# Optimization experiments

Hardware: AMD Instinct MI355X
Metric: run time of the kernel (lower is better)

## Reference

```python
import jax, jax.numpy as jnp
import numpy as np

N = 10000; E = 320000
DIM = 176; ATT = 16; SH_HEADS = 16; TH = 4; NH = SH_HEADS + TH; VD = DIM // SH_HEADS
LMAX = 3; NSPH = (LMAX + 1) ** 2; ZDIM = 16; RDIM = 16
RSTART = 0.8; CUT = 5.0; NLAYERS = 2


def _ln(x):
    mu = jnp.mean(x, axis=-1, keepdims=True)
    dx = x - mu
    var = jnp.mean(dx ** 2, axis=-1, keepdims=True)
    return dx * (1e-6 + var) ** (-0.5)


def _sph(v):
    # real spherical harmonics up to l=3, unnormalized overall scale, [E,16]
    x, y, z = v[..., 0], v[..., 1], v[..., 2]
    s3 = np.float32(np.sqrt(3.0)); s15 = np.float32(np.sqrt(15.0))
    c1 = np.float32(np.sqrt(5.0 / 8.0)); c2 = np.float32(np.sqrt(3.0 / 8.0))
    x2, y2, z2 = x * x, y * y, z * z
    return jnp.stack([
        jnp.ones_like(x),
        x, y, z,
        s3 * x * y, s3 * y * z, 0.5 * (3.0 * z2 - 1.0), s3 * x * z, 0.5 * s3 * (x2 - y2),
        c1 * y * (3.0 * x2 - y2), s15 * x * y * z, c2 * y * (5.0 * z2 - 1.0),
        0.5 * z * (5.0 * z2 - 3.0), c2 * x * (5.0 * z2 - 1.0),
        0.5 * s15 * z * (x2 - y2), c1 * x * (x2 - 3.0 * y2),
    ], axis=-1)


def setup_inputs() -> dict:
    key = jax.random.key(0)
    ks = jax.random.split(key, 32)

    def rn(k, shape):
        fan_in = shape[0] if len(shape) > 1 else shape[0]
        return jax.random.normal(k, shape, dtype=jnp.float32) / np.float32(np.sqrt(shape[0]))

    species = jax.random.randint(ks[0], (N,), 0, 64)
    edge_src = jax.random.randint(ks[1], (E,), 0, N)
    edge_dst = jax.random.randint(ks[2], (E,), 0, N)
    distances = RSTART + (CUT - RSTART) * jax.random.uniform(ks[3], (E,), dtype=jnp.float32)
    raw = jax.random.normal(ks[4], (E, 3), dtype=jnp.float32)
    dirn = raw / jnp.linalg.norm(raw, axis=-1, keepdims=True)
    vec = dirn * distances[:, None]
    switch = 0.5 * (jnp.cos(jnp.pi * distances / CUT) + 1.0)

    inp = {
        'species': species, 'distances': distances, 'switch': switch,
        'edge_src': edge_src, 'edge_dst': edge_dst, 'vec': vec,
        'z_table': jax.random.normal(ks[5], (64, ZDIM), dtype=jnp.float32),
        'w_species': rn(ks[6], (ZDIM, DIM)),
        'pos_w1_0': rn(ks[7], (RDIM, 2 * ATT)), 'pos_b1_0': jnp.zeros((2 * ATT,), jnp.float32),
        'pos_w2_0': rn(ks[8], (2 * ATT, ATT)), 'pos_b2_0': jnp.zeros((ATT,), jnp.float32),
        'wq_0': rn(ks[9], (DIM, NH * ATT)), 'wk_0': rn(ks[10], (DIM, NH * ATT)),
        'wv_0': rn(ks[11], (DIM, SH_HEADS * VD)),
        'upd_w_0': rn(ks[12], (2 * DIM, DIM)), 'upd_b_0': jnp.zeros((DIM,), jnp.float32),
        'pos_w1_1': rn(ks[13], (RDIM + TH * (LMAX + 1), 2 * ATT)), 'pos_b1_1': jnp.zeros((2 * ATT,), jnp.float32),
        'pos_w2_1': rn(ks[14], (2 * ATT, ATT)), 'pos_b2_1': jnp.zeros((ATT,), jnp.float32),
        'wq_1': rn(ks[15], (DIM, NH * ATT)), 'wk_1': rn(ks[16], (DIM, NH * ATT)),
        'wv_1': rn(ks[17], (DIM, SH_HEADS * VD)),
        'upd_w_1': rn(ks[18], (2 * DIM, DIM)), 'upd_b_1': jnp.zeros((DIM,), jnp.float32),
    }
    return inp


def reference(species, distances, switch, edge_src, edge_dst, vec,
              z_table, w_species,
              pos_w1_0, pos_b1_0, pos_w2_0, pos_b2_0, wq_0, wk_0, wv_0, upd_w_0, upd_b_0,
              pos_w1_1, pos_b1_1, pos_w2_1, pos_b2_1, wq_1, wk_1, wv_1, upd_w_1, upd_b_1):
    Nn = species.shape[0]
    Zi = z_table[species]                      # [N, ZDIM] species encoding
    xi = _ln(Zi @ w_species)                   # [N, DIM]

    vhat = vec / distances[:, None]
    Yij = _sph(vhat)                           # [E, NSPH]
    ls = np.repeat(np.arange(LMAX + 1), 2 * np.arange(LMAX + 1) + 1)
    parity = jnp.asarray(((-1.0) ** ls).astype(np.float32))  # [NSPH]

    centers = jnp.linspace(RSTART, CUT, RDIM, dtype=jnp.float32)
    sigma = np.float32((CUT - RSTART) / (RDIM - 1))
    radial = jnp.exp(-(((distances[:, None] - centers) / sigma) ** 2))  # [E, RDIM]

    Vi = jnp.zeros((Nn, TH, NSPH), jnp.float32)
    pos = [(pos_w1_0, pos_b1_0, pos_w2_0, pos_b2_0), (pos_w1_1, pos_b1_1, pos_w2_1, pos_b2_1)]
    att = [(wq_0, wk_0, wv_0, upd_w_0, upd_b_0), (wq_1, wk_1, wv_1, upd_w_1, upd_b_1)]
    inv_sqrt_d = np.float32(1.0 / np.sqrt(ATT))

    for layer in range(NLAYERS):
        pw1, pb1, pw2, pb2 = pos[layer]
        wq, wk, wv, uw, ub = att[layer]
        if layer == 0:
            ur = radial
        else:
            # tensor relative positional features: [E, TH, NSPH]
            xij2 = (Vi[edge_dst] + (parity * Vi)[edge_src]) * Yij[:, None, :]
            us = [xij2[:, :, l * l:(l + 1) * (l + 1)].sum(axis=-1) for l in range(LMAX + 1)]
            ur = jnp.concatenate([radial] + us, axis=-1)
        w = jax.nn.swish(ur @ pw1 + pb1) @ pw2 + pb2     # [E, ATT] positional encoding
        q = (xi @ wq).reshape(Nn, NH, ATT)
        k = (xi @ wk).reshape(Nn, NH, ATT)
        # multiplicative relative positional attention coefficients [E, NH]
        aij = jnp.einsum('ehd,ed->eh', q[edge_dst] * k[edge_src], w) * (switch[:, None] * inv_sqrt_d)
        a_s, a_t = aij[:, :SH_HEADS], aij[:, SH_HEADS:]
        v = (xi @ wv).reshape(Nn, SH_HEADS, VD)
        mi = jax.ops.segment_sum(a_s[:, :, None] * v[edge_src], edge_dst, num_segments=Nn)  # [N,SH,VD]
        Vi = Vi + jax.ops.segment_sum(
            a_t[:, :, None] * (Yij[:, None, :] + parity * Vi[edge_src]), edge_dst, num_segments=Nn)
        ui = jnp.concatenate([xi, mi.reshape(Nn, -1)], axis=-1)
        xi = _ln(xi + ui @ uw + ub)
    return xi
```

## Files before the change

### kernel.cpp

```cpp
#include <hip/hip_runtime.h>
#include <hip/hip_bf16.h>
#include <math.h>

#define N_NODES 10000
#define N_PAD   10048
#define N_EDGES 320000
#define DIM     176
#define ATT     16
#define SH_HEADS 16
#define THH     4
#define NH      20
#define VD      11
#define ZDIM    16
#define RDIM    16
#define QK_W    (NH*ATT)
#define QKV_W   816
#define UI_W    (2*DIM)
#define KQ      192
#define SIGINV  3.5714285714285716f
#define RSTEP   0.28f

typedef unsigned short ushort_t;
typedef __attribute__((ext_vector_type(8))) short bf16x8;
typedef __attribute__((ext_vector_type(4))) float f32x4;


__device__ __forceinline__ ushort_t f2bf(float f) {
    __hip_bfloat16 b = __float2bfloat16(f);
    return *(ushort_t*)&b;
}

__device__ __forceinline__ float bf2f(ushort_t u) {
    return __uint_as_float(((unsigned)u) << 16);
}

__device__ __forceinline__ void sph16(float x, float y, float z, float* Y) {
    const float s3  = 1.7320508075688772f;
    const float s15 = 3.872983346207417f;
    const float c1  = 0.7905694150420949f;
    const float c2  = 0.6123724356957945f;
    float x2 = x*x, y2 = y*y, z2 = z*z;
    Y[0]  = 1.0f;
    Y[1]  = x;
    Y[2]  = y;
    Y[3]  = z;
    Y[4]  = s3 * x * y;
    Y[5]  = s3 * y * z;
    Y[6]  = 0.5f * (3.0f * z2 - 1.0f);
    Y[7]  = s3 * x * z;
    Y[8]  = 0.5f * s3 * (x2 - y2);
    Y[9]  = c1 * y * (3.0f * x2 - y2);
    Y[10] = s15 * x * y * z;
    Y[11] = c2 * y * (5.0f * z2 - 1.0f);
    Y[12] = 0.5f * z * (5.0f * z2 - 3.0f);
    Y[13] = c2 * x * (5.0f * z2 - 1.0f);
    Y[14] = 0.5f * s15 * z * (x2 - y2);
    Y[15] = c1 * x * (x2 - 3.0f * y2);
}

__device__ __forceinline__ void unpack8(const uint4 u, float* f) {
    f[0] = __uint_as_float(u.x << 16);
    f[1] = __uint_as_float(u.x & 0xffff0000u);
    f[2] = __uint_as_float(u.y << 16);
    f[3] = __uint_as_float(u.y & 0xffff0000u);
    f[4] = __uint_as_float(u.z << 16);
    f[5] = __uint_as_float(u.z & 0xffff0000u);
    f[6] = __uint_as_float(u.w << 16);
    f[7] = __uint_as_float(u.w & 0xffff0000u);
}


__global__ __launch_bounds__(256) void k_deg(const int* edst, int* deg, int* rank) {
    int e = blockIdx.x * 256 + threadIdx.x;
    if (e < N_EDGES) rank[e] = atomicAdd(&deg[edst[e]], 1);
}

__global__ __launch_bounds__(1024) void k_scan1(const int* deg, int* incl, int* bsum) {
    __shared__ int sd[1024];
    int b = blockIdx.x, tid = threadIdx.x;
    int gi = b * 1024 + tid;
    int v = (gi < N_NODES) ? deg[gi] : 0;
    sd[tid] = v;
    __syncthreads();
    for (int s = 1; s < 1024; s <<= 1) {
        int add = (tid >= s) ? sd[tid - s] : 0;
        __syncthreads();
        sd[tid] += add;
        __syncthreads();
    }
    if (gi < N_NODES) incl[gi] = sd[tid];
    if (tid == 1023) bsum[b] = sd[1023];
}

__global__ __launch_bounds__(1024) void k_scan3(const int* deg, const int* incl, const int* bsum,
                                                int* off) {
    __shared__ int bpre_s;
    int b = blockIdx.x, tid = threadIdx.x;
    if (tid == 0) {
        int acc = 0;
        for (int k = 0; k < b; k++) acc += bsum[k];
        bpre_s = acc;
    }
    __syncthreads();
    int gi = b * 1024 + tid;
    if (gi < N_NODES) {
        off[gi + 1] = bpre_s + incl[gi];
    }
    if (gi == 0) off[0] = 0;
}

__global__ __launch_bounds__(256) void k_perm(const int* edst, const int* rank,
                                              const int* off, int* perm) {
    int e = blockIdx.x * 256 + threadIdx.x;
    if (e >= N_EDGES) return;
    perm[off[edst[e]] + rank[e]] = e;
}

__global__ __launch_bounds__(256) void k_build(const int* __restrict__ perm,
        const int* __restrict__ esrc, const int* __restrict__ edst,
        const float* __restrict__ dist, const float* __restrict__ swit,
        const float* __restrict__ vec,
        int* src_c, int* dst_c, float* dist_c, float* sc_c, float* Yf) {
    int p = blockIdx.x * 256 + threadIdx.x;
    if (p >= N_EDGES) return;
    int e  = perm[p];
    int s  = esrc[e];
    int t_ = edst[e];
    float d  = dist[e];
    float sw = swit[e];
    float vx = vec[(size_t)e*3 + 0];
    float vy = vec[(size_t)e*3 + 1];
    float vz = vec[(size_t)e*3 + 2];
    float inv = 1.0f / d;
    vx *= inv; vy *= inv; vz *= inv;
    src_c[p]  = s;
    dst_c[p]  = t_;
    dist_c[p] = d;
    sc_c[p]   = sw * 0.25f;
    float Y[16];
    sph16(vx, vy, vz, Y);
    #pragma unroll
    for (int m = 0; m < 16; m += 4)
        *(float4*)&Yf[(size_t)p * 16 + m] = make_float4(Y[m], Y[m+1], Y[m+2], Y[m+3]);
}


__device__ __forceinline__ void prep_qkv_body(int bid, int tid, const float* wq,
        const float* wk, const float* wv, ushort_t* Wtq) {
    int id = bid * 256 + tid;
    if (id >= 832 * KQ) return;
    int n = id / KQ, k = id - (id / KQ) * KQ;
    float v = 0.0f;
    if (k < DIM && n < QKV_W)
        v = (n < 320) ? wq[k * 320 + n] : (n < 640) ? wk[k * 320 + (n - 320)]
                                                    : wv[k * DIM + (n - 640)];
    Wtq[id] = f2bf(v);
}

__device__ __forceinline__ void prep_upd_body(int bid, int tid, const float* uw, ushort_t* Wtu) {
    int id = bid * 256 + tid;
    if (id >= 192 * UI_W) return;
    int n = id / UI_W, k = id - (id / UI_W) * UI_W;
    float v = (n < DIM) ? uw[k * DIM + n] : 0.0f;
    Wtu[id] = f2bf(v);
}

__device__ __forceinline__ void prep_mlp_body(int bid, int tid, const float* pw1,
        const float* pw2, ushort_t* w1T, ushort_t* w2T, int K1) {
    int id = bid * 256 + tid;
    if (id < 1024) {
        int n = id >> 5, k = id & 31;
        w1T[n * 32 + k] = (k < K1) ? f2bf(pw1[k * 32 + n]) : 0;
    } else if (id < 1536) {
        int id2 = id - 1024;
        int n = id2 >> 5, k = id2 & 31;
        w2T[n * 32 + k] = f2bf(pw2[k * 16 + n]);
    }
}

__global__ __launch_bounds__(256) void k_prep_all(
        const float* wq0, const float* wk0, const float* wv0, ushort_t* Wtq0,
        const float* wq1, const float* wk1, const float* wv1, ushort_t* Wtq1,
        const float* uw0, ushort_t* Wtu0, const float* uw1, ushort_t* Wtu1,
        const float* pw1_0, const float* pw2_0, ushort_t* w1T0, ushort_t* w2T0,
        const float* pw1_1, const float* pw2_1, ushort_t* w1T1, ushort_t* w2T1) {
    int bid = blockIdx.x, tid = threadIdx.x;
    if (bid < 624)        prep_qkv_body(bid,        tid, wq0, wk0, wv0, Wtq0);
    else if (bid < 1248)  prep_qkv_body(bid - 624,  tid, wq1, wk1, wv1, Wtq1);
    else if (bid < 1512)  prep_upd_body(bid - 1248, tid, uw0, Wtu0);
    else if (bid < 1776)  prep_upd_body(bid - 1512, tid, uw1, Wtu1);
    else if (bid < 1782)  prep_mlp_body(bid - 1776, tid, pw1_0, pw2_0, w1T0, w2T0, 16);
    else if (bid < 1788)  prep_mlp_body(bid - 1782, tid, pw1_1, pw2_1, w1T1, w2T1, 32);
}


template<int KCHUNKS, int OMODE>
__global__ __launch_bounds__(256) void k_gemm(const ushort_t* __restrict__ A, int sA,
                                              const ushort_t* __restrict__ Bt, int sB,
                                              void* __restrict__ Cv, int sC, int M, int N,
                                              ushort_t* __restrict__ qh,
                                              ushort_t* __restrict__ kh,
                                              ushort_t* __restrict__ vh) {
    __shared__ ushort_t As[64 * 40];
    __shared__ ushort_t Bs[64 * 40];
    int tid  = threadIdx.x;
    int m0   = blockIdx.y * 64, n0 = blockIdx.x * 64;
    int w    = tid >> 6, lane = tid & 63, quad = lane >> 4, c16 = lane & 15;
    int arow = tid >> 2, aseg = tid & 3;
    f32x4 acc[4] = {};
    for (int kc = 0; kc < KCHUNKS; kc++) {
        int k0 = kc * 32;
        *(uint4*)&As[arow * 40 + aseg * 8] =
            *(const uint4*)&A[(size_t)(m0 + arow) * sA + k0 + aseg * 8];
        *(uint4*)&Bs[arow * 40 + aseg * 8] =
            *(const uint4*)&Bt[(size_t)(n0 + arow) * sB + k0 + aseg * 8];
        __syncthreads();
        bf16x8 a = *(const bf16x8*)&As[(w * 16 + c16) * 40 + quad * 8];
        #pragma unroll
        for (int t = 0; t < 4; t++) {
            bf16x8 b = *(const bf16x8*)&Bs[(t * 16 + c16) * 40 + quad * 8];
            acc[t] = __builtin_amdgcn_mfma_f32_16x16x32_bf16(a, b, acc[t], 0, 0, 0);
        }
        __syncthreads();
    }
    #pragma unroll
    for (int t = 0; t < 4; t++) {
        #pragma unroll
        for (int r = 0; r < 4; r++) {
            int row = m0 + w * 16 + quad * 4 + r;
            int col = n0 + t * 16 + c16;
            if (row < M && col < N) {
                if (OMODE == 1) {
                    ushort_t bv = f2bf(acc[t][r]);
                    if (col < 320)      qh[(size_t)row * QK_W + col] = bv;
                    else if (col < 640) kh[(size_t)row * QK_W + (col - 320)] = bv;
                    else                vh[(size_t)row * DIM  + (col - 640)] = bv;
                } else {
                    ((float*)Cv)[(size_t)row * sC + col] = acc[t][r];
                }
            }
        }
    }
}


__global__ __launch_bounds__(256) void k_node_init(const int* species, const float* z_table,
                                                   const float* wsp, float* xi,
                                                   ushort_t* xib, ushort_t* cxm) {
    __shared__ float zs[16 * ZDIM];
    __shared__ float yt[16 * DIM];
    __shared__ float red[256];
    __shared__ float mus[16], rstds[16];
    int base = blockIdx.x * 16;
    int tid  = threadIdx.x;
    { int n = tid >> 4, kk = tid & 15;
      zs[tid] = z_table[species[base + n] * ZDIM + kk]; }
    __syncthreads();
    int c = tid;
    if (c < DIM) {
        float acc[16];
        #pragma unroll
        for (int n = 0; n < 16; n++) acc[n] = 0.0f;
        for (int kk = 0; kk < ZDIM; kk++) {
            float w = wsp[kk * DIM + c];
            #pragma unroll
            for (int n = 0; n < 16; n++) acc[n] += zs[n * ZDIM + kk] * w;
        }
        #pragma unroll
        for (int n = 0; n < 16; n++) yt[n * DIM + c] = acc[n];
    }
    __syncthreads();
    { int n2 = tid >> 4, j = tid & 15;
      float s = 0.0f;
      for (int c2 = j; c2 < DIM; c2 += 16) s += yt[n2 * DIM + c2];
      red[tid] = s; }
    __syncthreads();
    if (tid < 16) { float s = 0; for (int j = 0; j < 16; j++) s += red[tid * 16 + j]; mus[tid] = s / (float)DIM; }
    __syncthreads();
    { int n2 = tid >> 4, j = tid & 15;
      float mu = mus[n2], s = 0.0f;
      for (int c2 = j; c2 < DIM; c2 += 16) { float d = yt[n2 * DIM + c2] - mu; s += d * d; }
      red[tid] = s; }
    __syncthreads();
    if (tid < 16) { float s = 0; for (int j = 0; j < 16; j++) s += red[tid * 16 + j]; rstds[tid] = rsqrtf(s / (float)DIM + 1e-6f); }
    __syncthreads();
    if (c < DIM) {
        #pragma unroll
        for (int n = 0; n < 16; n++) {
            float val = (yt[n * DIM + c] - mus[n]) * rstds[n];
            xi[(size_t)(base + n) * DIM + c] = val;
            ushort_t bv = f2bf(val);
            xib[(size_t)(base + n) * KQ + c]   = bv;
            cxm[(size_t)(base + n) * UI_W + c] = bv;
        }
    } else if (c < KQ) {
        #pragma unroll
        for (int n = 0; n < 16; n++) xib[(size_t)(base + n) * KQ + c] = 0;
    }
}


template<bool L0>
__global__ __launch_bounds__(256) void k_edge(const float* dist_c, const float* sc_c,
        const int* src_c, const int* dst_c, const float* Yf, const ushort_t* Vih,
        const ushort_t* qh, const ushort_t* kh,
        const ushort_t* w1T, const float* pb1, const ushort_t* w2T, const float* pb2,
        ushort_t* aijh) {
    __shared__ ushort_t urS[64 * 40];
    __shared__ ushort_t Ht[4][16 * 40];
    __shared__ float    wdS[64 * 17];
    __shared__ ushort_t aS[NH][64];
    int tid  = threadIdx.x;
    int w    = tid >> 6, lane = tid & 63, quad = lane >> 4, c16 = lane & 15;
    int eb   = blockIdx.x * 64;

    int le = tid >> 2, part = tid & 3;
    int ie = eb + le;
    int sE = src_c[ie], tE = dst_c[ie];

    if (!L0) {
        int e  = tid & 63, tp = tid >> 6;
        int i  = eb + e;
        float d = dist_c[i];
        ushort_t ur4[4];
        #pragma unroll
        for (int r0 = 0; r0 < 4; r0++) {
            int r = tp * 4 + r0;
            float cc = 0.8f + (float)r * RSTEP;
            float uu = (d - cc) * SIGINV;
            ur4[r0] = f2bf(__expf(-uu * uu));
        }
        *(uint2*)&urS[e * 40 + tp * 4] = *(uint2*)ur4;
        float Y[16];
        #pragma unroll
        for (int m = 0; m < 16; m += 4) {
            float4 y = *(const float4*)&Yf[(size_t)i * 16 + m];
            Y[m] = y.x; Y[m+1] = y.y; Y[m+2] = y.z; Y[m+3] = y.w;
        }
        int s = src_c[i], t_ = dst_c[i];
        const uint4* vd4 = (const uint4*)(Vih + (size_t)t_ * 64);
        const uint4* vs4 = (const uint4*)(Vih + (size_t)s  * 64);
        int th = tp;
        float fd[16], fs[16];
        unpack8(vd4[2*th],   fd);     unpack8(vd4[2*th+1], fd+8);
        unpack8(vs4[2*th],   fs);     unpack8(vs4[2*th+1], fs+8);
        float us0 = (fd[0] + fs[0]) * Y[0];
        float us1 = 0.0f, us2 = 0.0f, us3 = 0.0f;
        #pragma unroll
        for (int m = 1; m < 4; m++)  us1 += (fd[m] - fs[m]) * Y[m];
        #pragma unroll
        for (int m = 4; m < 9; m++)  us2 += (fd[m] + fs[m]) * Y[m];
        #pragma unroll
        for (int m = 9; m < 16; m++) us3 += (fd[m] - fs[m]) * Y[m];
        urS[e * 40 + 16 + 0 * 4 + th] = f2bf(us0);
        urS[e * 40 + 16 + 1 * 4 + th] = f2bf(us1);
        urS[e * 40 + 16 + 2 * 4 + th] = f2bf(us2);
        urS[e * 40 + 16 + 3 * 4 + th] = f2bf(us3);
        __syncthreads();
    }

    uint4 kr[10];
    {
        const uint4* kseg = (const uint4*)(kh + (size_t)sE * QK_W) + part * 10;
        #pragma unroll
        for (int j = 0; j < 10; j++) kr[j] = kseg[j];
    }

    {
        int e0 = eb + w * 16;
        bf16x8 a1;
        if (L0) {
            float d = dist_c[e0 + c16];
            #pragma unroll
            for (int j = 0; j < 8; j++) {
                int r = quad * 8 + j;
                float v = 0.0f;
                if (r < 16) { float cc = 0.8f + (float)r * RSTEP; float uu = (d - cc) * SIGINV; v = __expf(-uu * uu); }
                a1[j] = (short)f2bf(v);
            }
        } else {
            a1 = *(const bf16x8*)&urS[(w * 16 + c16) * 40 + quad * 8];
        }
        bf16x8 b0 = *(const bf16x8*)&w1T[c16 * 32 + quad * 8];
        bf16x8 b1 = *(const bf16x8*)&w1T[(16 + c16) * 32 + quad * 8];
        f32x4 acc0 = {}, acc1 = {};
        acc0 = __builtin_amdgcn_mfma_f32_16x16x32_bf16(a1, b0, acc0, 0, 0, 0);
        acc1 = __builtin_amdgcn_mfma_f32_16x16x32_bf16(a1, b1, acc1, 0, 0, 0);
        float bb0 = pb1[c16], bb1 = pb1[c16 + 16];
        #pragma unroll
        for (int r = 0; r < 4; r++) {
            int er = quad * 4 + r;
            float h0 = acc0[r] + bb0; h0 = h0 / (1.0f + __expf(-h0));
            float h1 = acc1[r] + bb1; h1 = h1 / (1.0f + __expf(-h1));
            Ht[w][er * 40 + c16]      = f2bf(h0);
            Ht[w][er * 40 + 16 + c16] = f2bf(h1);
        }
        __syncthreads();
        bf16x8 a2 = *(const bf16x8*)&Ht[w][c16 * 40 + quad * 8];
        bf16x8 b2 = *(const bf16x8*)&w2T[c16 * 32 + quad * 8];
        f32x4 acc2 = {};
        acc2 = __builtin_amdgcn_mfma_f32_16x16x32_bf16(a2, b2, acc2, 0, 0, 0);
        float bb2 = pb2[c16];
        #pragma unroll
        for (int r = 0; r < 4; r++) {
            int er = quad * 4 + r;
            wdS[(w * 16 + er) * 17 + c16] = (acc2[r] + bb2) * sc_c[e0 + er];
        }
    }
    __syncthreads();

    {
        float wd[16];
        #pragma unroll
        for (int p = 0; p < 16; p++) wd[p] = wdS[le * 17 + p];
        const uint4* q4 = (const uint4*)(qh + (size_t)tE * QK_W) + part * 10;
        #pragma unroll
        for (int j = 0; j < 5; j++) {
            int h = part * 5 + j;
            float qa[8], qb[8], ka[8], kb[8];
            unpack8(q4[2*j],   qa); unpack8(q4[2*j+1], qb);
            unpack8(kr[2*j],   ka); unpack8(kr[2*j+1], kb);
            float acc = 0.0f;
            #pragma unroll
            for (int dd = 0; dd < 8; dd++) acc += qa[dd] * ka[dd] * wd[dd];
            #pragma unroll
            for (int dd = 0; dd < 8; dd++) acc += qb[dd] * kb[dd] * wd[8 + dd];
            aS[h][le] = f2bf(acc);
        }
    }
    __syncthreads();
    {
        const uint* aSw = (const uint*)aS;
        for (int idx = tid; idx < NH * 32; idx += 256) {
            int h = idx >> 5, w2 = idx & 31;
            *(uint*)(aijh + (size_t)h * N_EDGES + eb + w2 * 2) = aSw[h * 32 + w2];
        }
    }
}


__device__ __forceinline__ void mi_step(int i, int c0, bool f1, bool f2,
        const int* src_c, const ushort_t* aA, const ushort_t* aB, const ushort_t* vh,
        float& acc0, float& acc1, float& acc2, float& acc3) {
    int s0 = src_c[i];
    uint2 v0 = *(const uint2*)(vh + (size_t)s0 * DIM + c0);
    float a00 = bf2f(aA[i]), a0B = bf2f(aB[i]);
    float g01 = f1 ? a0B : a00, g02 = f2 ? a0B : a00;
    acc0 += a00 * __uint_as_float(v0.x << 16);
    acc1 += g01 * __uint_as_float(v0.x & 0xffff0000u);
    acc2 += g02 * __uint_as_float(v0.y << 16);
    acc3 += a0B * __uint_as_float(v0.y & 0xffff0000u);
}

__device__ __forceinline__ void mi_wave(int n, int lane, const int* off, const int* src_c,
        const ushort_t* aijh, const ushort_t* vh, ushort_t* cxm) {
    if (lane >= 44) return;
    int c0 = lane * 4;
    int hA = c0 / VD;
    int hB = (c0 + 3) / VD;
    bool f1 = ((c0 + 1) / VD) != hA;
    bool f2 = ((c0 + 2) / VD) != hA;
    const ushort_t* aA = aijh + (size_t)hA * N_EDGES;
    const ushort_t* aB = aijh + (size_t)hB * N_EDGES;
    int start = off[n], end = off[n + 1];
    float acc0 = 0, acc1 = 0, acc2 = 0, acc3 = 0;
    int cnt = end - start;
    int i = start;

#define MI_ACC(vv, av, bv) { \
    float aa = bf2f(av), ab = bf2f(bv); \
    float g1 = f1 ? ab : aa, g2 = f2 ? ab : aa; \
    acc0 += aa * __uint_as_float((vv).x << 16); \
    acc1 += g1 * __uint_as_float((vv).x & 0xffff0000u); \
    acc2 += g2 * __uint_as_float((vv).y << 16); \
    acc3 += ab * __uint_as_float((vv).y & 0xffff0000u); }

    if (cnt >= 4) {
        int iend = start + (cnt & ~3);
        int s0 = src_c[i], s1 = src_c[i+1], s2 = src_c[i+2], s3 = src_c[i+3];
        uint2 v0 = *(const uint2*)(vh + (size_t)s0 * DIM + c0);
        uint2 v1 = *(const uint2*)(vh + (size_t)s1 * DIM + c0);
        uint2 v2 = *(const uint2*)(vh + (size_t)s2 * DIM + c0);
        uint2 v3 = *(const uint2*)(vh + (size_t)s3 * DIM + c0);
        ushort_t pA0 = aA[i], pA1 = aA[i+1], pA2 = aA[i+2], pA3 = aA[i+3];
        ushort_t pB0 = aB[i], pB1 = aB[i+1], pB2 = aB[i+2], pB3 = aB[i+3];
        for (i += 4; i + 4 <= iend; i += 4) {
            int t0 = src_c[i], t1 = src_c[i+1], t2 = src_c[i+2], t3 = src_c[i+3];
            uint2 w0 = *(const uint2*)(vh + (size_t)t0 * DIM + c0);
            uint2 w1 = *(const uint2*)(vh + (size_t)t1 * DIM + c0);
            uint2 w2 = *(const uint2*)(vh + (size_t)t2 * DIM + c0);
            uint2 w3 = *(const uint2*)(vh + (size_t)t3 * DIM + c0);
            ushort_t qA0 = aA[i], qA1 = aA[i+1], qA2 = aA[i+2], qA3 = aA[i+3];
            ushort_t qB0 = aB[i], qB1 = aB[i+1], qB2 = aB[i+2], qB3 = aB[i+3];
            MI_ACC(v0, pA0, pB0); MI_ACC(v1, pA1, pB1);
            MI_ACC(v2, pA2, pB2); MI_ACC(v3, pA3, pB3);
            v0 = w0; v1 = w1; v2 = w2; v3 = w3;
            pA0 = qA0; pA1 = qA1; pA2 = qA2; pA3 = qA3;
            pB0 = qB0; pB1 = qB1; pB2 = qB2; pB3 = qB3;
        }
        MI_ACC(v0, pA0, pB0); MI_ACC(v1, pA1, pB1);
        MI_ACC(v2, pA2, pB2); MI_ACC(v3, pA3, pB3);
    }
    for (; i < end; i++)
        mi_step(i, c0, f1, f2, src_c, aA, aB, vh, acc0, acc1, acc2, acc3);
#undef MI_ACC
    ushort_t o[4] = {f2bf(acc0), f2bf(acc1), f2bf(acc2), f2bf(acc3)};
    *(uint2*)(cxm + (size_t)n * UI_W + DIM + c0) = *(uint2*)o;
}

__device__ __forceinline__ void vi_wave(int n, int lane, const int* off,
        const float* Yf, const ushort_t* aijh, ushort_t* Vih) {
    int th = lane >> 4, sm = lane & 15;
    const ushort_t* ah = aijh + (size_t)(SH_HEADS + th) * N_EDGES;
    int start = off[n], end = off[n + 1];
    float acc = 0.0f;
    int cnt = end - start;
    int i = start;
    if (cnt >= 4) {
        int iend = start + (cnt & ~3);
        float a0 = bf2f(ah[i]),   y0 = Yf[(size_t)i * 16 + sm];
        float a1 = bf2f(ah[i+1]), y1 = Yf[(size_t)(i+1) * 16 + sm];
        float a2 = bf2f(ah[i+2]), y2 = Yf[(size_t)(i+2) * 16 + sm];
        float a3 = bf2f(ah[i+3]), y3 = Yf[(size_t)(i+3) * 16 + sm];
        for (i += 4; i + 4 <= iend; i += 4) {
            float b0 = bf2f(ah[i]),   z0 = Yf[(size_t)i * 16 + sm];
            float b1 = bf2f(ah[i+1]), z1 = Yf[(size_t)(i+1) * 16 + sm];
            float b2 = bf2f(ah[i+2]), z2 = Yf[(size_t)(i+2) * 16 + sm];
            float b3 = bf2f(ah[i+3]), z3 = Yf[(size_t)(i+3) * 16 + sm];
            acc += a0 * y0 + a1 * y1 + a2 * y2 + a3 * y3;
            a0 = b0; a1 = b1; a2 = b2; a3 = b3;
            y0 = z0; y1 = z1; y2 = z2; y3 = z3;
        }
        acc += a0 * y0 + a1 * y1 + a2 * y2 + a3 * y3;
    }
    for (; i < end; i++)
        acc += bf2f(ah[i]) * Yf[(size_t)i * 16 + sm];
    Vih[(size_t)n * 64 + lane] = f2bf(acc);
}

__global__ __launch_bounds__(256) void k_agg0(const int* off, const int* src_c,
        const float* Yf, const ushort_t* aijh, const ushort_t* vh,
        ushort_t* cxm, ushort_t* Vih) {
    int wid  = blockIdx.x * 4 + (threadIdx.x >> 6);
    int lane = threadIdx.x & 63;
    if (wid < N_NODES)
        mi_wave(wid, lane, off, src_c, aijh, vh, cxm);
    else
        vi_wave(wid - N_NODES, lane, off, Yf, aijh, Vih);
}

__global__ __launch_bounds__(256) void k_agg1(const int* off, const int* src_c,
        const ushort_t* aijh, const ushort_t* vh, ushort_t* cxm) {
    int wid  = blockIdx.x * 4 + (threadIdx.x >> 6);
    int lane = threadIdx.x & 63;
    mi_wave(wid, lane, off, src_c, aijh, vh, cxm);
}


__global__ __launch_bounds__(256) void k_lnfinal(const float* yg, const float* xi,
        const float* ub, float* xo, ushort_t* xib, ushort_t* cxm) {
    __shared__ float yt[16 * DIM];
    __shared__ float red[256];
    __shared__ float mus[16], rstds[16];
    int base = blockIdx.x * 16;
    int tid  = threadIdx.x;
    for (int idx = tid; idx < 16 * DIM; idx += 256) {
        int n = idx / DIM, c = idx - n * DIM;
        yt[idx] = xi[(size_t)(base + n) * DIM + c]
                + yg[(size_t)(base + n) * DIM + c] + ub[c];
    }
    __syncthreads();
    { int n2 = tid >> 4, j = tid & 15;
      float s = 0.0f;
      for (int c2 = j; c2 < DIM; c2 += 16) s += yt[n2 * DIM + c2];
      red[tid] = s; }
    __syncthreads();
    if (tid < 16) { float s = 0; for (int j = 0; j < 16; j++) s += red[tid * 16 + j]; mus[tid] = s / (float)DIM; }
    __syncthreads();
    { int n2 = tid >> 4, j = tid & 15;
      float mu = mus[n2], s = 0.0f;
      for (int c2 = j; c2 < DIM; c2 += 16) { float d = yt[n2 * DIM + c2] - mu; s += d * d; }
      red[tid] = s; }
    __syncthreads();
    if (tid < 16) { float s = 0; for (int j = 0; j < 16; j++) s += red[tid * 16 + j]; rstds[tid] = rsqrtf(s / (float)DIM + 1e-6f); }
    __syncthreads();
    int c = tid;
    if (c < DIM) {
        #pragma unroll
        for (int n = 0; n < 16; n++) {
            float val = (yt[n * DIM + c] - mus[n]) * rstds[n];
            xo[(size_t)(base + n) * DIM + c] = val;
            ushort_t bv = f2bf(val);
            xib[(size_t)(base + n) * KQ + c]   = bv;
            cxm[(size_t)(base + n) * UI_W + c] = bv;
        }
    } else if (c < KQ) {
        #pragma unroll
        for (int n = 0; n < 16; n++) xib[(size_t)(base + n) * KQ + c] = 0;
    }
}


extern "C" void kernel_launch(void* const* d_in, const int* in_sizes, int n_in,
                              void* d_out, int out_size, void* d_ws, size_t ws_size,
                              hipStream_t stream) {
    const int*   species = (const int*)  d_in[0];
    const float* dist    = (const float*)d_in[1];
    const float* swit    = (const float*)d_in[2];
    const int*   esrc    = (const int*)  d_in[3];
    const int*   edst    = (const int*)  d_in[4];
    const float* vec     = (const float*)d_in[5];
    const float* z_table = (const float*)d_in[6];
    const float* wsp     = (const float*)d_in[7];
    const float* pw1_0 = (const float*)d_in[8],  *pb1_0 = (const float*)d_in[9];
    const float* pw2_0 = (const float*)d_in[10], *pb2_0 = (const float*)d_in[11];
    const float* wq0 = (const float*)d_in[12], *wk0 = (const float*)d_in[13];
    const float* wv0 = (const float*)d_in[14], *uw0 = (const float*)d_in[15];
    const float* ub0 = (const float*)d_in[16];
    const float* pw1_1 = (const float*)d_in[17], *pb1_1 = (const float*)d_in[18];
    const float* pw2_1 = (const float*)d_in[19], *pb2_1 = (const float*)d_in[20];
    const float* wq1 = (const float*)d_in[21], *wk1 = (const float*)d_in[22];
    const float* wv1 = (const float*)d_in[23], *uw1 = (const float*)d_in[24];
    const float* ub1 = (const float*)d_in[25];
    float* out = (float*)d_out;

    char* p = (char*)d_ws;
    auto alloc = [&](size_t bytes) -> char* {
        char* r = p;
        p += (bytes + 255) & ~(size_t)255;
        return r;
    };
    int* deg    = (int*)alloc((size_t)N_NODES * 4);
    int* incl   = (int*)alloc((size_t)N_NODES * 4);
    int* bsum   = (int*)alloc(64);
    int* off    = (int*)alloc((size_t)(N_NODES + 1) * 4);
    int* rank   = (int*)alloc((size_t)N_EDGES * 4);
    int* perm   = (int*)alloc((size_t)N_EDGES * 4);
    int*   src_c  = (int*)  alloc((size_t)N_EDGES * 4);
    int*   dst_c  = (int*)  alloc((size_t)N_EDGES * 4);
    float* dist_c = (float*)alloc((size_t)N_EDGES * 4);
    float* sc_c   = (float*)alloc((size_t)N_EDGES * 4);
    float* Yf     = (float*)alloc((size_t)N_EDGES * 16 * 4);
    float* xiA  = (float*)alloc((size_t)N_NODES * DIM * 4);
    float* xiB  = (float*)alloc((size_t)N_NODES * DIM * 4);
    ushort_t* xib  = (ushort_t*)alloc((size_t)N_PAD * KQ * 2);
    ushort_t* cxm  = (ushort_t*)alloc((size_t)N_PAD * UI_W * 2);
    ushort_t* qh   = (ushort_t*)alloc((size_t)N_NODES * QK_W * 2);
    ushort_t* kh   = (ushort_t*)alloc((size_t)N_NODES * QK_W * 2);
    ushort_t* vh   = (ushort_t*)alloc((size_t)N_NODES * DIM * 2);
    float* ybuf    = (float*)alloc((size_t)N_NODES * DIM * 4);
    ushort_t* Wtq0 = (ushort_t*)alloc((size_t)832 * KQ * 2);
    ushort_t* Wtq1 = (ushort_t*)alloc((size_t)832 * KQ * 2);
    ushort_t* Wtu0 = (ushort_t*)alloc((size_t)192 * UI_W * 2);
    ushort_t* Wtu1 = (ushort_t*)alloc((size_t)192 * UI_W * 2);
    ushort_t* w1T0 = (ushort_t*)alloc((size_t)32 * 32 * 2);
    ushort_t* w2T0 = (ushort_t*)alloc((size_t)16 * 32 * 2);
    ushort_t* w1T1 = (ushort_t*)alloc((size_t)32 * 32 * 2);
    ushort_t* w2T1 = (ushort_t*)alloc((size_t)16 * 32 * 2);
    ushort_t* Vih  = (ushort_t*)alloc((size_t)N_NODES * 64 * 2);
    ushort_t* aijh = (ushort_t*)alloc((size_t)N_EDGES * NH * 2);

    const int NB_E  = (N_EDGES + 255) / 256;
    const int NB_F  = N_EDGES / 64;
    const int NB_T  = N_NODES / 16;
    const dim3 GRID_QKV(13, 157);
    const dim3 GRID_UPD(3, 157);

    hipMemsetAsync(deg, 0, (size_t)N_NODES * 4, stream);
    k_deg<<<NB_E, 256, 0, stream>>>(edst, deg, rank);
    k_scan1<<<10, 1024, 0, stream>>>(deg, incl, bsum);
    k_scan3<<<10, 1024, 0, stream>>>(deg, incl, bsum, off);
    k_perm<<<NB_E, 256, 0, stream>>>(edst, rank, off, perm);
    k_build<<<NB_E, 256, 0, stream>>>(perm, esrc, edst, dist, swit, vec,
                                      src_c, dst_c, dist_c, sc_c, Yf);

    k_prep_all<<<1788, 256, 0, stream>>>(wq0, wk0, wv0, Wtq0, wq1, wk1, wv1, Wtq1,
                                         uw0, Wtu0, uw1, Wtu1,
                                         pw1_0, pw2_0, w1T0, w2T0,
                                         pw1_1, pw2_1, w1T1, w2T1);

    k_node_init<<<NB_T, 256, 0, stream>>>(species, z_table, wsp, xiA, xib, cxm);

    k_gemm<6, 1><<<GRID_QKV, 256, 0, stream>>>(xib, KQ, Wtq0, KQ, nullptr, 0,
                                               N_NODES, QKV_W, qh, kh, vh);
    k_edge<true><<<NB_F, 256, 0, stream>>>(dist_c, sc_c, src_c, dst_c, Yf, Vih,
                                           qh, kh, w1T0, pb1_0, w2T0, pb2_0, aijh);
    k_agg0<<<5000, 256, 0, stream>>>(off, src_c, Yf, aijh, vh, cxm, Vih);
    k_gemm<11, 0><<<GRID_UPD, 256, 0, stream>>>(cxm, UI_W, Wtu0, UI_W, ybuf, DIM,
                                                N_NODES, DIM, nullptr, nullptr, nullptr);
    k_lnfinal<<<NB_T, 256, 0, stream>>>(ybuf, xiA, ub0, xiB, xib, cxm);

    k_gemm<6, 1><<<GRID_QKV, 256, 0, stream>>>(xib, KQ, Wtq1, KQ, nullptr, 0,
                                               N_NODES, QKV_W, qh, kh, vh);
    k_edge<false><<<NB_F, 256, 0, stream>>>(dist_c, sc_c, src_c, dst_c, Yf, Vih,
                                            qh, kh, w1T1, pb1_1, w2T1, pb2_1, aijh);
    k_agg1<<<2500, 256, 0, stream>>>(off, src_c, aijh, vh, cxm);
    k_gemm<11, 0><<<GRID_UPD, 256, 0, stream>>>(cxm, UI_W, Wtu1, UI_W, ybuf, DIM,
                                                N_NODES, DIM, nullptr, nullptr, nullptr);
    k_lnfinal<<<NB_T, 256, 0, stream>>>(ybuf, xiB, ub1, out, xib, cxm);
}
```

Baseline: 384.3 us.

## Pack per-edge inputs into 32-byte records and hoist key gather in edge kernel

k_deg now also writes each edge's src, dst, distance, switch and vector into a packed 32-byte record, so k_build's permuted gather pulls two contiguous uint4 loads per edge instead of seven scattered loads from separate arrays. Separately, k_edge issues its 10-vector key gather before the non-layer-0 tensor-feature block and its barrier, so that global load latency can overlap with that work. The cost is an extra 10 MB workspace write plus read, and kr stays live longer, which adds register pressure.

```diff
diff --git a/kernel.cpp b/kernel.cpp
--- a/kernel.cpp
+++ b/kernel.cpp
@@ -70,9 +70,25 @@
 }
 
 
-__global__ __launch_bounds__(256) void k_deg(const int* edst, int* deg, int* rank) {
+__global__ __launch_bounds__(256) void k_deg(const int* __restrict__ edst,
+        const int* __restrict__ esrc, const float* __restrict__ dist,
+        const float* __restrict__ swit, const float* __restrict__ vec,
+        int* deg, int* rank, uint4* pk) {
     int e = blockIdx.x * 256 + threadIdx.x;
-    if (e < N_EDGES) rank[e] = atomicAdd(&deg[edst[e]], 1);
+    if (e >= N_EDGES) return;
+    int t_ = edst[e];
+    rank[e] = atomicAdd(&deg[t_], 1);
+    uint4 a, b;
+    a.x = (unsigned)esrc[e];
+    a.y = (unsigned)t_;
+    a.z = __float_as_uint(dist[e]);
+    a.w = __float_as_uint(swit[e]);
+    b.x = __float_as_uint(vec[(size_t)e*3 + 0]);
+    b.y = __float_as_uint(vec[(size_t)e*3 + 1]);
+    b.z = __float_as_uint(vec[(size_t)e*3 + 2]);
+    b.w = 0u;
+    pk[(size_t)e*2 + 0] = a;
+    pk[(size_t)e*2 + 1] = b;
 }
 
 __global__ __launch_bounds__(1024) void k_scan1(const int* deg, int* incl, int* bsum) {
@@ -117,22 +133,21 @@
 }
 
 __global__ __launch_bounds__(256) void k_build(const int* __restrict__ perm,
-        const int* __restrict__ esrc, const int* __restrict__ edst,
-        const float* __restrict__ dist, const float* __restrict__ swit,
-        const float* __restrict__ vec,
+        const uint4* __restrict__ pk,
         int* src_c, int* dst_c, float* dist_c, float* sc_c, float* Yf) {
     int p = blockIdx.x * 256 + threadIdx.x;
     if (p >= N_EDGES) return;
     int e  = perm[p];
-    int s  = esrc[e];
-    int t_ = edst[e];
-    float d  = dist[e];
-    float sw = swit[e];
-    float vx = vec[(size_t)e*3 + 0];
-    float vy = vec[(size_t)e*3 + 1];
-    float vz = vec[(size_t)e*3 + 2];
+    uint4 a = pk[(size_t)e*2 + 0];
+    uint4 b = pk[(size_t)e*2 + 1];
+    int s  = (int)a.x;
+    int t_ = (int)a.y;
+    float d  = __uint_as_float(a.z);
+    float sw = __uint_as_float(a.w);
     float inv = 1.0f / d;
-    vx *= inv; vy *= inv; vz *= inv;
+    float vx = __uint_as_float(b.x) * inv;
+    float vy = __uint_as_float(b.y) * inv;
+    float vz = __uint_as_float(b.z) * inv;
     src_c[p]  = s;
     dst_c[p]  = t_;
     dist_c[p] = d;
@@ -318,6 +333,13 @@
     int ie = eb + le;
     int sE = src_c[ie], tE = dst_c[ie];
 
+    uint4 kr[10];
+    {
+        const uint4* kseg = (const uint4*)(kh + (size_t)sE * QK_W) + part * 10;
+        #pragma unroll
+        for (int j = 0; j < 10; j++) kr[j] = kseg[j];
+    }
+
     if (!L0) {
         int e  = tid & 63, tp = tid >> 6;
         int i  = eb + e;
@@ -357,13 +379,6 @@
         urS[e * 40 + 16 + 2 * 4 + th] = f2bf(us2);
         urS[e * 40 + 16 + 3 * 4 + th] = f2bf(us3);
         __syncthreads();
-    }
-
-    uint4 kr[10];
-    {
-        const uint4* kseg = (const uint4*)(kh + (size_t)sE * QK_W) + part * 10;
-        #pragma unroll
-        for (int j = 0; j < 10; j++) kr[j] = kseg[j];
     }
 
     {
@@ -636,6 +651,7 @@
     int* off    = (int*)alloc((size_t)(N_NODES + 1) * 4);
     int* rank   = (int*)alloc((size_t)N_EDGES * 4);
     int* perm   = (int*)alloc((size_t)N_EDGES * 4);
+    uint4* pk   = (uint4*)alloc((size_t)N_EDGES * 32);
     int*   src_c  = (int*)  alloc((size_t)N_EDGES * 4);
     int*   dst_c  = (int*)  alloc((size_t)N_EDGES * 4);
     float* dist_c = (float*)alloc((size_t)N_EDGES * 4);
@@ -667,12 +683,11 @@
     const dim3 GRID_UPD(3, 157);
 
     hipMemsetAsync(deg, 0, (size_t)N_NODES * 4, stream);
-    k_deg<<<NB_E, 256, 0, stream>>>(edst, deg, rank);
+    k_deg<<<NB_E, 256, 0, stream>>>(edst, esrc, dist, swit, vec, deg, rank, pk);
     k_scan1<<<10, 1024, 0, stream>>>(deg, incl, bsum);
     k_scan3<<<10, 1024, 0, stream>>>(deg, incl, bsum, off);
     k_perm<<<NB_E, 256, 0, stream>>>(edst, rank, off, perm);
-    k_build<<<NB_E, 256, 0, stream>>>(perm, esrc, edst, dist, swit, vec,
-                                      src_c, dst_c, dist_c, sc_c, Yf);
+    k_build<<<NB_E, 256, 0, stream>>>(perm, pk, src_c, dst_c, dist_c, sc_c, Yf);
 
     k_prep_all<<<1788, 256, 0, stream>>>(wq0, wk0, wv0, Wtq0, wq1, wk1, wv1, Wtq1,
                                          uw0, Wtu0, uw1, Wtu1,
```

Measured after the change: 381.5 us. No clear change (-0.7%).
